# Optimization experiments

Hardware: AMD Instinct MI355X
Metric: run time of the kernel (lower is better)

Reference implementation:

```python
import jax, jax.numpy as jnp
import numpy as np
import math
from jax import lax

B, HS, WS, C, T, TD, HH, TOPM = 8, 64, 64, 512, 77, 512, 8, 3
DH = C // HH
CONF_TH = 0.35


def _layernorm(x, w, b, eps=1e-5):
    mu = x.mean(-1, keepdims=True)
    var = ((x - mu) ** 2).mean(-1, keepdims=True)
    return (x - mu) * lax.rsqrt(var + eps) * w + b


def _l2norm(x, eps=1e-6):
    n = jnp.sqrt((x * x).sum(-1, keepdims=True))
    return x / jnp.maximum(n, eps)


def _forward(visual_features, text_features, geo_mask,
             ln1_w, ln1_b, wq, bq, wk, bk, wv, bv, wo, bo,
             gate_w, gate_b, logit_scale, alpha,
             ln2_w, ln2_b, ffn_w1, ffn_b1, ffn_w2, ffn_b2):
    Bb, Hs, Ws, Cv = visual_features.shape
    N = Hs * Ws
    # Pre-LN + flatten spatial
    x = _layernorm(visual_features, ln1_w, ln1_b).reshape(Bb, N, Cv)
    q_full = x @ wq + bq                                  # [B,N,C]
    pad_mask = jnp.abs(text_features).sum(-1) <= 1e-6     # [B,T]
    k_full = text_features @ wk + bk                      # [B,T,C]
    v_full = text_features @ wv + bv
    # per-token L2 normalize over full channel dim, then split heads
    q = _l2norm(q_full).reshape(Bb, N, HH, DH)
    k = _l2norm(k_full).reshape(Bb, T, HH, DH)
    v = v_full.reshape(Bb, T, HH, DH)
    scale = jnp.exp(jnp.clip(logit_scale, -2.0, 2.0)) / jnp.sqrt(jnp.float32(DH))
    sim = jnp.einsum('bnhd,bthd->bnht', q, k) * scale     # [B,N,H,T]
    # geo gate (4D tensor branch): log-bias on logits + multiplicative channel gate later
    gate_map = jnp.clip(geo_mask, 0.3, 1.0)               # [B,1,Hs,Ws]
    geo_gate_flat = gate_map.reshape(Bb, N, 1)            # [B,N,1]
    sim = sim + jnp.log(jnp.maximum(gate_map.reshape(Bb, N), 1e-6))[:, :, None, None]
    sim = jnp.where(pad_mask[:, None, None, :], -jnp.inf, sim)
    # Top-K sparsification before softmax (threshold at the K-th value)
    topv = lax.top_k(sim, TOPM)[0]                        # [B,N,H,K]
    sim = jnp.where(sim >= topv[..., -1:], sim, -jnp.inf)
    attn = jax.nn.softmax(sim, axis=-1)
    attn = attn / jnp.maximum(attn.sum(-1, keepdims=True), 1e-6)
    # fully-padded rows -> zero
    all_pad = pad_mask.all(axis=1)
    attn = jnp.where(all_pad[:, None, None, None], 0.0, attn)
    # confidence bypass: conf = max_prob * (1 - normalized entropy), mean over heads
    a_hn = attn.transpose(0, 2, 1, 3)                     # [B,H,N,T]
    maxp = a_hn.max(-1, keepdims=True)
    t_eff = jnp.maximum((a_hn > 0).astype(a_hn.dtype).sum(-1, keepdims=True), 2.0)
    p = jnp.maximum(a_hn, 1e-8)
    ent = jnp.maximum(-(p * jnp.log(p)).sum(-1, keepdims=True) / jnp.log(t_eff), 0.0)
    conf = jnp.clip(maxp * (1.0 - ent), 0.0, 1.0).mean(axis=1)   # [B,N,1]
    conf_scale = CONF_TH + (1.0 - CONF_TH) * jnp.clip(conf, 0.0, 1.0)
    aligned = jnp.einsum('bnht,bthd->bnhd', attn, v).reshape(Bb, N, HH * DH)
    aligned = (aligned @ wo + bo) * conf_scale
    gate = jax.nn.sigmoid(x @ gate_w + gate_b) * geo_gate_flat
    y = x + alpha * gate * aligned
    h = _layernorm(y, ln2_w, ln2_b)
    y = y + (jax.nn.gelu(h @ ffn_w1 + ffn_b1, approximate=False) @ ffn_w2 + ffn_b2)
    return y.reshape(Bb, Hs, Ws, Cv)


def setup_inputs() -> dict:
    key = jax.random.key(0)
    ks = jax.random.split(key, 16)
    def w(k, shp, fan_in):
        return (jax.random.normal(k, shp, jnp.float32) * (1.0 / math.sqrt(fan_in))).astype(jnp.float32)
    return {
        'visual_features': jax.random.normal(ks[0], (B, HS, WS, C), jnp.float32),
        'text_features':   jax.random.normal(ks[1], (B, T, TD), jnp.float32),
        'geo_mask':        jax.random.uniform(ks[2], (B, 1, HS, WS), jnp.float32),
        'ln1_w': jnp.ones((C,), jnp.float32), 'ln1_b': jnp.zeros((C,), jnp.float32),
        'wq': w(ks[3], (C, C), C),   'bq': jnp.zeros((C,), jnp.float32),
        'wk': w(ks[4], (TD, C), TD), 'bk': jnp.zeros((C,), jnp.float32),
        'wv': w(ks[5], (TD, C), TD), 'bv': jnp.zeros((C,), jnp.float32),
        'wo': w(ks[6], (C, C), C),   'bo': jnp.zeros((C,), jnp.float32),
        'gate_w': w(ks[7], (C, C), C), 'gate_b': jnp.zeros((C,), jnp.float32),
        'logit_scale': jnp.float32(math.log(1.0 / 0.07)),
        'alpha': jnp.float32(0.1),
        'ln2_w': jnp.ones((C,), jnp.float32), 'ln2_b': jnp.zeros((C,), jnp.float32),
        'ffn_w1': w(ks[8], (C, 4 * C), C),    'ffn_b1': jnp.zeros((4 * C,), jnp.float32),
        'ffn_w2': w(ks[9], (4 * C, C), 4 * C), 'ffn_b2': jnp.zeros((C,), jnp.float32),
    }


def reference(visual_features, text_features, geo_mask,
              ln1_w, ln1_b, wq, bq, wk, bk, wv, bv, wo, bo,
              gate_w, gate_b, logit_scale, alpha,
              ln2_w, ln2_b, ffn_w1, ffn_b1, ffn_w2, ffn_b2):
    return _forward(visual_features, text_features, geo_mask,
                    ln1_w, ln1_b, wq, bq, wk, bk, wv, bv, wo, bo,
                    gate_w, gate_b, logit_scale, alpha,
                    ln2_w, ln2_b, ffn_w1, ffn_b1, ffn_w2, ffn_b2)
```

## Files before the change

### kernel.cpp

```cpp
#include <hip/hip_runtime.h>
#include <hip/hip_bf16.h>
#include <math.h>

#define TT 77
#define MTOT 32768

typedef __attribute__((ext_vector_type(8))) short bf16x8;
typedef __attribute__((ext_vector_type(4))) float floatx4;

#define GPTR(p) ((const __attribute__((address_space(1))) void*)(p))
#define LPTR(p) ((__attribute__((address_space(3))) void*)(p))

__device__ __forceinline__ float wred_sum(float v) {
#pragma unroll
  for (int o = 32; o >= 1; o >>= 1) v += __shfl_xor(v, o, 64);
  return v;
}

__device__ __forceinline__ unsigned short f2bf(float f) {
  unsigned int u = __float_as_uint(f);
  unsigned int r = (u + 0x7fffu + ((u >> 16) & 1u)) >> 16;
  return (unsigned short)r;
}
__device__ __forceinline__ float bf2f(unsigned short h) {
  return __uint_as_float(((unsigned int)h) << 16);
}
__device__ __forceinline__ unsigned int cvt2bf(float a, float b) {
  unsigned int r;
  asm("v_cvt_pk_bf16_f32 %0, %1, %2" : "=v"(r) : "v"(a), "v"(b));
  return r;
}

__device__ __forceinline__ float fast_gelu(float o) {
  const float z = fabsf(o) * 0.70710678118654752f;
  const float t = __builtin_amdgcn_rcpf(fmaf(0.3275911f, z, 1.0f));
  float p = fmaf(1.061405429f, t, -1.453152027f);
  p = fmaf(p, t, 1.421413741f);
  p = fmaf(p, t, -0.284496736f);
  p = fmaf(p, t, 0.254829592f);
  p = p * t;
  const float erfz = fmaf(-p, __expf(-z * z), 1.0f);
  const float s = __builtin_copysignf(erfz, o);
  return 0.5f * o * (1.0f + s);
}

__device__ __forceinline__ float fast_sigmoid(float o) {
  return __builtin_amdgcn_rcpf(1.0f + __expf(-o));
}

__global__ __launch_bounds__(256)
void ln_bf16_kernel(const float* __restrict__ in, const float* __restrict__ gw,
                    const float* __restrict__ gb, unsigned short* __restrict__ out) {
  const int wv = threadIdx.x >> 6, lane = threadIdx.x & 63;
  const size_t row = (size_t)blockIdx.x * 4 + wv;
  const float* p = in + row * 512 + lane * 8;
  float4 a = *(const float4*)p;
  float4 b = *(const float4*)(p + 4);
  float s = a.x + a.y + a.z + a.w + b.x + b.y + b.z + b.w;
  float mu = wred_sum(s) * (1.0f / 512.0f);
  float d[8] = {a.x - mu, a.y - mu, a.z - mu, a.w - mu,
                b.x - mu, b.y - mu, b.z - mu, b.w - mu};
  float ss = 0.f;
#pragma unroll
  for (int i = 0; i < 8; ++i) ss = fmaf(d[i], d[i], ss);
  float var = wred_sum(ss) * (1.0f / 512.0f);
  float rstd = rsqrtf(var + 1e-5f);
  float4 w0 = *(const float4*)(gw + lane * 8);
  float4 w1 = *(const float4*)(gw + lane * 8 + 4);
  float4 c0 = *(const float4*)(gb + lane * 8);
  float4 c1 = *(const float4*)(gb + lane * 8 + 4);
  float o[8];
  o[0] = d[0] * rstd * w0.x + c0.x;  o[1] = d[1] * rstd * w0.y + c0.y;
  o[2] = d[2] * rstd * w0.z + c0.z;  o[3] = d[3] * rstd * w0.w + c0.w;
  o[4] = d[4] * rstd * w1.x + c1.x;  o[5] = d[5] * rstd * w1.y + c1.y;
  o[6] = d[6] * rstd * w1.z + c1.z;  o[7] = d[7] * rstd * w1.w + c1.w;
  __align__(16) unsigned short ob[8];
#pragma unroll
  for (int i = 0; i < 8; ++i) ob[i] = f2bf(o[i]);
  *(uint4*)(out + row * 512 + lane * 8) = *(const uint4*)ob;
}

__global__ __launch_bounds__(256)
void zero_acc_kernel(float* __restrict__ ssq, float* __restrict__ conf) {
  const int i = blockIdx.x * 256 + threadIdx.x;
  ssq[i] = 0.0f;
  conf[i] = 0.0f;
}

__global__ __launch_bounds__(256)
void transpose_bf16_kernel(const float* __restrict__ W, unsigned short* __restrict__ WTb,
                           int K, int N) {
  __shared__ float s[32][33];
  const int tx = threadIdx.x & 31, ty = threadIdx.x >> 5;
  const int n0 = blockIdx.x * 32, k0 = blockIdx.y * 32;
#pragma unroll
  for (int j = 0; j < 4; ++j)
    s[ty + 8 * j][tx] = W[(size_t)(k0 + ty + 8 * j) * N + n0 + tx];
  __syncthreads();
#pragma unroll
  for (int j = 0; j < 4; ++j)
    WTb[(size_t)(n0 + ty + 8 * j) * K + k0 + tx] = f2bf(s[tx][ty + 8 * j]);
}

__global__ __launch_bounds__(256)
void transpose_pair_kernel(const float* __restrict__ W,
                           unsigned short* __restrict__ WTh,
                           unsigned short* __restrict__ WTl, int K, int N) {
  __shared__ float s[32][33];
  const int tx = threadIdx.x & 31, ty = threadIdx.x >> 5;
  const int n0 = blockIdx.x * 32, k0 = blockIdx.y * 32;
#pragma unroll
  for (int j = 0; j < 4; ++j)
    s[ty + 8 * j][tx] = W[(size_t)(k0 + ty + 8 * j) * N + n0 + tx];
  __syncthreads();
#pragma unroll
  for (int j = 0; j < 4; ++j) {
    const float a = s[tx][ty + 8 * j];
    const unsigned short hi = f2bf(a);
    WTh[(size_t)(n0 + ty + 8 * j) * K + k0 + tx] = hi;
    WTl[(size_t)(n0 + ty + 8 * j) * K + k0 + tx] = f2bf(a - bf2f(hi));
  }
}

__global__ __launch_bounds__(256)
void text_cvt_kernel(const float* __restrict__ text,
                     unsigned short* __restrict__ thi,
                     unsigned short* __restrict__ tlo,
                     float* __restrict__ negm) {
  const int wv = threadIdx.x >> 6, lane = threadIdx.x & 63;
  const int row = blockIdx.x * 4 + wv;
  if (row >= 616) {
    const uint4 z = {0u, 0u, 0u, 0u};
    *(uint4*)(thi + (size_t)row * 512 + lane * 8) = z;
    *(uint4*)(tlo + (size_t)row * 512 + lane * 8) = z;
    return;
  }
  const float* p = text + (size_t)row * 512 + lane * 8;
  float4 a = *(const float4*)p;
  float4 b = *(const float4*)(p + 4);
  float v[8] = {a.x, a.y, a.z, a.w, b.x, b.y, b.z, b.w};
  float ab = 0.f;
#pragma unroll
  for (int i = 0; i < 8; ++i) ab += fabsf(v[i]);
  ab = wred_sum(ab);
  __align__(16) unsigned short hb[8];
  __align__(16) unsigned short lb[8];
#pragma unroll
  for (int i = 0; i < 8; ++i) {
    hb[i] = f2bf(v[i]);
    lb[i] = f2bf(v[i] - bf2f(hb[i]));
  }
  *(uint4*)(thi + (size_t)row * 512 + lane * 8) = *(const uint4*)hb;
  *(uint4*)(tlo + (size_t)row * 512 + lane * 8) = *(const uint4*)lb;
  if (lane == 0) {
    const int bb = row / 77, t = row - bb * 77;
    negm[bb * 80 + t] = (ab <= 1e-6f) ? -INFINITY : 0.0f;
  }
}

__global__ __launch_bounds__(256)
void kv_gemm(const unsigned short* __restrict__ AH,
             const unsigned short* __restrict__ AL,
             const unsigned short* __restrict__ BH,
             const unsigned short* __restrict__ BL,
             const float* __restrict__ bk, const float* __restrict__ bv,
             float* __restrict__ outp) {
  const int K = 512;
  __shared__ __align__(16) unsigned short AsH[128 * 32];
  __shared__ __align__(16) unsigned short AsL[128 * 32];
  __shared__ __align__(16) unsigned short BsH[128 * 32];
  __shared__ __align__(16) unsigned short BsL[128 * 32];
  const int tid = threadIdx.x;
  const int wid = tid >> 6, lane = tid & 63;
  const int wr = wid >> 1, wc = wid & 1;
  const int m16 = lane & 15, quad = lane >> 4;
  const int row0 = blockIdx.y * 128, col0 = blockIdx.x * 128;

  const floatx4 zero4 = {0.f, 0.f, 0.f, 0.f};
  floatx4 acc[4][4];
#pragma unroll
  for (int i = 0; i < 4; ++i)
#pragma unroll
    for (int j = 0; j < 4; ++j) acc[i][j] = zero4;

  const int srow = tid >> 2;
  const int schunk = (tid & 3) ^ (srow & 3);
  const unsigned short* AgH = AH + (size_t)(row0 + srow) * K + schunk * 8;
  const unsigned short* AgL = AL + (size_t)(row0 + srow) * K + schunk * 8;
  const unsigned short* BgH = BH + (size_t)(col0 + srow) * K + schunk * 8;
  const unsigned short* BgL = BL + (size_t)(col0 + srow) * K + schunk * 8;
  char* AsHB = (char*)AsH + tid * 16;
  char* AsLB = (char*)AsL + tid * 16;
  char* BsHB = (char*)BsH + tid * 16;
  char* BsLB = (char*)BsL + tid * 16;
  const int rq = quad ^ (m16 & 3);
  const int aOfs = (wr * 64 + m16) * 32 + rq * 8;
  const int bOfs = (wc * 64 + m16) * 32 + rq * 8;

  for (int k0 = 0; k0 < K; k0 += 32) {
    __syncthreads();
    __builtin_amdgcn_global_load_lds(GPTR(AgH + k0), LPTR(AsHB), 16, 0, 0);
    __builtin_amdgcn_global_load_lds(GPTR(AgH + (size_t)64 * K + k0), LPTR(AsHB + 4096), 16, 0, 0);
    __builtin_amdgcn_global_load_lds(GPTR(AgL + k0), LPTR(AsLB), 16, 0, 0);
    __builtin_amdgcn_global_load_lds(GPTR(AgL + (size_t)64 * K + k0), LPTR(AsLB + 4096), 16, 0, 0);
    __builtin_amdgcn_global_load_lds(GPTR(BgH + k0), LPTR(BsHB), 16, 0, 0);
    __builtin_amdgcn_global_load_lds(GPTR(BgH + (size_t)64 * K + k0), LPTR(BsHB + 4096), 16, 0, 0);
    __builtin_amdgcn_global_load_lds(GPTR(BgL + k0), LPTR(BsLB), 16, 0, 0);
    __builtin_amdgcn_global_load_lds(GPTR(BgL + (size_t)64 * K + k0), LPTR(BsLB + 4096), 16, 0, 0);
    __syncthreads();
    bf16x8 afH[4], afL[4], bfH[4], bfL[4];
#pragma unroll
    for (int i = 0; i < 4; ++i) {
      afH[i] = *(const bf16x8*)(AsH + aOfs + i * 16 * 32);
      afL[i] = *(const bf16x8*)(AsL + aOfs + i * 16 * 32);
      bfH[i] = *(const bf16x8*)(BsH + bOfs + i * 16 * 32);
      bfL[i] = *(const bf16x8*)(BsL + bOfs + i * 16 * 32);
    }
#pragma unroll
    for (int mi = 0; mi < 4; ++mi)
#pragma unroll
      for (int ni = 0; ni < 4; ++ni) {
        acc[mi][ni] = __builtin_amdgcn_mfma_f32_16x16x32_bf16(afH[mi], bfH[ni], acc[mi][ni], 0, 0, 0);
        acc[mi][ni] = __builtin_amdgcn_mfma_f32_16x16x32_bf16(afH[mi], bfL[ni], acc[mi][ni], 0, 0, 0);
        acc[mi][ni] = __builtin_amdgcn_mfma_f32_16x16x32_bf16(afL[mi], bfH[ni], acc[mi][ni], 0, 0, 0);
      }
  }

  const float* bp = (col0 < 512) ? bk : bv;
  const int cbase = (col0 < 512) ? col0 : col0 - 512;
  float bb[4];
#pragma unroll
  for (int ni = 0; ni < 4; ++ni) bb[ni] = bp[cbase + wc * 64 + ni * 16 + m16];
#pragma unroll
  for (int mi = 0; mi < 4; ++mi)
#pragma unroll
    for (int r = 0; r < 4; ++r) {
      const int row = row0 + wr * 64 + mi * 16 + quad * 4 + r;
#pragma unroll
      for (int ni = 0; ni < 4; ++ni) {
        const int col = col0 + wc * 64 + ni * 16 + m16;
        outp[(size_t)row * 1024 + col] = acc[mi][ni][r] + bb[ni];
      }
    }
}

__global__ __launch_bounds__(256)
void knorm_kernel(const float* __restrict__ KV,
                  unsigned short* __restrict__ khb) {
  const int wv = threadIdx.x >> 6, lane = threadIdx.x & 63;
  const int row = blockIdx.x * 4 + wv;
  const float* p = KV + (size_t)row * 1024 + lane * 8;
  float4 a = *(const float4*)p;
  float4 b = *(const float4*)(p + 4);
  float v[8] = {a.x, a.y, a.z, a.w, b.x, b.y, b.z, b.w};
  float ss = 0.f;
#pragma unroll
  for (int i = 0; i < 8; ++i) ss = fmaf(v[i], v[i], ss);
  ss = wred_sum(ss);
  const float sc = 1.0f / fmaxf(sqrtf(ss), 1e-6f);
  const int bb = row / 77, t = row - bb * 77;
  const int c = lane * 8, h = c >> 6, d = c & 63;
  __align__(16) unsigned short ob[8];
#pragma unroll
  for (int i = 0; i < 8; ++i) ob[i] = f2bf(v[i] * sc);
  *(uint4*)(khb + (((size_t)bb * 8 + h) * 80 + t) * 64 + d) = *(const uint4*)ob;
}

__global__ __launch_bounds__(256)
void kpad_zero_kernel(unsigned short* __restrict__ khb, float* __restrict__ negm) {
  const int i = blockIdx.x * 256 + threadIdx.x;
  const int bh = i / 192, rem = i - bh * 192;
  const int t = 77 + rem / 64, d = rem & 63;
  khb[(((size_t)bh) * 80 + t) * 64 + d] = 0;
  if (i < 24) negm[(i / 3) * 80 + 77 + (i % 3)] = -INFINITY;
}

__global__ __launch_bounds__(256)
void sim_attn_kernel(const unsigned short* __restrict__ qnb,
                     const unsigned short* __restrict__ khb,
                     const float* __restrict__ negm,
                     const float* __restrict__ ssq,
                     const float* __restrict__ logit_scale,
                     const float* __restrict__ vf,
                     unsigned short* __restrict__ alignedb,
                     float* __restrict__ confacc) {
  __shared__ __align__(16) char lbuf[128 * 81 * 4];
  unsigned short* As = (unsigned short*)lbuf;
  unsigned short* Bs = As + 128 * 72;
  float* simt = (float*)lbuf;

  const int bh = blockIdx.y;
  const int b = bh >> 3, h = bh & 7;
  const int row0 = blockIdx.x * 128;
  const int tid = threadIdx.x;

  {
    const int r = tid >> 1, half = tid & 1;
    const unsigned short* src = qnb + ((size_t)b * 4096 + row0 + r) * 512 + h * 64 + half * 32;
    unsigned short* dst = As + r * 72 + half * 32;
    *(uint4*)dst = *(const uint4*)src;
    *(uint4*)(dst + 8) = *(const uint4*)(src + 8);
    *(uint4*)(dst + 16) = *(const uint4*)(src + 16);
    *(uint4*)(dst + 24) = *(const uint4*)(src + 24);
  }
  if (tid < 160) {
    const int r = tid >> 1, half = tid & 1;
    const unsigned short* src = khb + ((size_t)bh * 80 + r) * 64 + half * 32;
    unsigned short* dst = Bs + r * 72 + half * 32;
    *(uint4*)dst = *(const uint4*)src;
    *(uint4*)(dst + 8) = *(const uint4*)(src + 8);
    *(uint4*)(dst + 16) = *(const uint4*)(src + 16);
    *(uint4*)(dst + 24) = *(const uint4*)(src + 24);
  }
  __syncthreads();

  const int w = tid >> 6, lane = tid & 63;
  const int m16 = lane & 15, quad = lane >> 4;
  const unsigned short* aBase = As + (w * 32 + m16) * 72 + quad * 8;
  const unsigned short* bBase = Bs + m16 * 72 + quad * 8;
  bf16x8 af[2][2], bf[5][2];
#pragma unroll
  for (int mi = 0; mi < 2; ++mi)
#pragma unroll
    for (int kk = 0; kk < 2; ++kk)
      af[mi][kk] = *(const bf16x8*)(aBase + mi * 16 * 72 + kk * 32);
#pragma unroll
  for (int ni = 0; ni < 5; ++ni)
#pragma unroll
    for (int kk = 0; kk < 2; ++kk)
      bf[ni][kk] = *(const bf16x8*)(bBase + ni * 16 * 72 + kk * 32);
  __syncthreads();

  const floatx4 zero4 = {0.f, 0.f, 0.f, 0.f};
  floatx4 acc[2][5];
#pragma unroll
  for (int mi = 0; mi < 2; ++mi)
#pragma unroll
    for (int ni = 0; ni < 5; ++ni) acc[mi][ni] = zero4;
#pragma unroll
  for (int kk = 0; kk < 2; ++kk)
#pragma unroll
    for (int mi = 0; mi < 2; ++mi)
#pragma unroll
      for (int ni = 0; ni < 5; ++ni)
        acc[mi][ni] = __builtin_amdgcn_mfma_f32_16x16x32_bf16(af[mi][kk], bf[ni][kk], acc[mi][ni], 0, 0, 0);

  const float ls = fminf(fmaxf(logit_scale[0], -2.0f), 2.0f);
  const float scale = expf(ls) * 0.125f;
  float nm[5];
#pragma unroll
  for (int ni = 0; ni < 5; ++ni) nm[ni] = negm[b * 80 + ni * 16 + m16];
#pragma unroll
  for (int mi = 0; mi < 2; ++mi)
#pragma unroll
    for (int r = 0; r < 4; ++r) {
      const int lr = w * 32 + quad * 4 + mi * 16 + r;
      const float ssv = ssq[(size_t)b * 4096 + row0 + lr];
      const float nsc = scale / fmaxf(sqrtf(ssv), 1e-6f);
#pragma unroll
      for (int ni = 0; ni < 5; ++ni)
        simt[lr * 81 + ni * 16 + m16] = acc[mi][ni][r] * nsc + nm[ni];
    }
  __syncthreads();

  const int lr = tid >> 1, half = tid & 1;
  const int n = row0 + lr;
  const float* sp = simt + lr * 81;

  float m1 = -INFINITY, m2 = -INFINITY, m3 = -INFINITY, m4 = -INFINITY;
  int a1 = 0, a2 = 0, a3 = 0;
  for (int t = 0; t < 80; ++t) {
    const float v = sp[t];
    const bool c1 = v > m1, c2 = v > m2, c3 = v > m3, c4 = v > m4;
    m4 = c4 ? (c3 ? m3 : v) : m4;
    m3 = c3 ? (c2 ? m2 : v) : m3;
    a3 = c3 ? (c2 ? a2 : t) : a3;
    m2 = c2 ? (c1 ? m1 : v) : m2;
    a2 = c2 ? (c1 ? a1 : t) : a2;
    m1 = c1 ? v : m1;
    a1 = c1 ? t : a1;
  }

  const bool dead = (m1 == -INFINITY);
  if (dead) m1 = 0.0f;
  const bool tie = (!dead) && ((m1 == m2) || (m2 == m3) || (m3 == m4));

  const float d2 = m2 - m1, d3 = m3 - m1;
  const float e2 = __expf(d2), e3 = __expf(d3);
  float s0 = 1.0f + e2 + e3;
  float s1 = ((e2 > 0.f) ? e2 * d2 : 0.f) + ((e3 > 0.f) ? e3 * d3 : 0.f);
  float cntf = 1.0f + ((e2 > 0.f) ? 1.f : 0.f) + ((e3 > 0.f) ? 1.f : 0.f);

  unsigned short* op = alignedb + ((size_t)b * 4096 + n) * 512 + h * 64 + half * 32;

  if (tie) {
    s0 = 0.f; s1 = 0.f; cntf = 0.f;
    float4 acc2[8];
#pragma unroll
    for (int i = 0; i < 8; ++i) acc2[i] = (float4){0.f, 0.f, 0.f, 0.f};
    for (int t = 0; t < 80; ++t) {
      const float v = sp[t];
      if (v >= m3) {
        const float e = expf(v - m1);
        if (e > 0.f) {
          s0 += e; s1 = fmaf(e, v - m1, s1); cntf += 1.f;
          const float4* vp = (const float4*)(vf + (size_t)(b * 77 + t) * 1024 + h * 64 + half * 32);
#pragma unroll
          for (int i = 0; i < 8; ++i) {
            const float4 x = vp[i];
            acc2[i].x = fmaf(e, x.x, acc2[i].x);
            acc2[i].y = fmaf(e, x.y, acc2[i].y);
            acc2[i].z = fmaf(e, x.z, acc2[i].z);
            acc2[i].w = fmaf(e, x.w, acc2[i].w);
          }
        }
      }
    }
    const float invt = 1.0f / s0;
#pragma unroll
    for (int i = 0; i < 4; ++i) {
      const float4 lo = acc2[2 * i], hi = acc2[2 * i + 1];
      uint4 pk;
      pk.x = cvt2bf(lo.x * invt, lo.y * invt);
      pk.y = cvt2bf(lo.z * invt, lo.w * invt);
      pk.z = cvt2bf(hi.x * invt, hi.y * invt);
      pk.w = cvt2bf(hi.z * invt, hi.w * invt);
      *(uint4*)(op + i * 8) = pk;
    }
  } else {
    const float inv0 = 1.0f / s0;
    const float wA = dead ? 0.f : inv0;
    const float wB = e2 * inv0, wC = e3 * inv0;
    const float* v1p = vf + (size_t)(b * 77 + a1) * 1024 + h * 64 + half * 32;
    const float* v2p = vf + (size_t)(b * 77 + a2) * 1024 + h * 64 + half * 32;
    const float* v3p = vf + (size_t)(b * 77 + a3) * 1024 + h * 64 + half * 32;
#pragma unroll
    for (int i = 0; i < 4; ++i) {
      const float4 x0 = ((const float4*)v1p)[2 * i];
      const float4 x1 = ((const float4*)v1p)[2 * i + 1];
      const float4 y0 = ((const float4*)v2p)[2 * i];
      const float4 y1 = ((const float4*)v2p)[2 * i + 1];
      const float4 z0 = ((const float4*)v3p)[2 * i];
      const float4 z1 = ((const float4*)v3p)[2 * i + 1];
      float4 r0, r1;
      r0.x = fmaf(wC, z0.x, fmaf(wB, y0.x, wA * x0.x));
      r0.y = fmaf(wC, z0.y, fmaf(wB, y0.y, wA * x0.y));
      r0.z = fmaf(wC, z0.z, fmaf(wB, y0.z, wA * x0.z));
      r0.w = fmaf(wC, z0.w, fmaf(wB, y0.w, wA * x0.w));
      r1.x = fmaf(wC, z1.x, fmaf(wB, y1.x, wA * x1.x));
      r1.y = fmaf(wC, z1.y, fmaf(wB, y1.y, wA * x1.y));
      r1.z = fmaf(wC, z1.z, fmaf(wB, y1.z, wA * x1.z));
      r1.w = fmaf(wC, z1.w, fmaf(wB, y1.w, wA * x1.w));
      uint4 pk;
      pk.x = cvt2bf(r0.x, r0.y);
      pk.y = cvt2bf(r0.z, r0.w);
      pk.z = cvt2bf(r1.x, r1.y);
      pk.w = cvt2bf(r1.z, r1.w);
      *(uint4*)(op + i * 8) = pk;
    }
  }

  if (half == 0) {
    const float inv = 1.0f / s0;
    const float entn = (__logf(s0) - s1 * inv) + (77.0f - cntf) * 1.8420681e-7f;
    const float ent = fmaxf(entn / __logf(fmaxf(cntf, 2.0f)), 0.0f);
    float conf_h = fminf(fmaxf(inv * (1.0f - ent), 0.0f), 1.0f);
    if (dead) conf_h = 0.f;
    atomicAdd(confacc + (size_t)b * 4096 + n, conf_h * 0.125f);
  }
}

template <int EPI, int KC>
__global__ __launch_bounds__(256)
void mfma_gemm(const unsigned short* __restrict__ A,
               const unsigned short* __restrict__ WT,
               const float* __restrict__ bias,
               void* __restrict__ outv, int M, int N,
               const unsigned short* __restrict__ e0b,
               const float* __restrict__ e1f,
               const float* __restrict__ e2f,
               const float* __restrict__ scf) {
  __shared__ __align__(16) unsigned short As[2][128 * 64];
  __shared__ __align__(16) unsigned short Bs[2][128 * 64];
  const int tid = threadIdx.x;
  const int wid = tid >> 6, lane = tid & 63;
  const int wr = wid >> 1, wc = wid & 1;
  const int m16 = lane & 15, quad = lane >> 4;

  const int nwg = gridDim.x * gridDim.y;
  const int orig = blockIdx.y * gridDim.x + blockIdx.x;
  const int qq = nwg >> 3, rr = nwg & 7;
  const int xcd = orig & 7, base = orig >> 3;
  const int logical = (xcd < rr ? xcd * (qq + 1) : rr * (qq + 1) + (xcd - rr) * qq) + base;
  const int bx = logical % gridDim.x, by = logical / gridDim.x;
  const int row0 = by * 128, col0 = bx * 128;

  const floatx4 zero4 = {0.f, 0.f, 0.f, 0.f};
  floatx4 acc[4][4];
#pragma unroll
  for (int i = 0; i < 4; ++i)
#pragma unroll
    for (int j = 0; j < 4; ++j) acc[i][j] = zero4;

  size_t aoff[4], boff[4];
  unsigned int ldso[4];
#pragma unroll
  for (int j = 0; j < 4; ++j) {
    const int s = wid * 64 + j * 256 + lane;
    const int r = s >> 3;
    const int gc = (s & 7) ^ (r & 7);
    aoff[j] = (size_t)(row0 + r) * KC + gc * 8;
    const int br = (r & 64) + 4 * (r & 15) + ((r >> 4) & 3);
    boff[j] = (size_t)(col0 + br) * KC + gc * 8;
    ldso[j] = (unsigned int)s * 16;
  }

  constexpr int NT = KC / 64;
#pragma unroll
  for (int j = 0; j < 4; ++j) {
    __builtin_amdgcn_global_load_lds(GPTR(A + aoff[j]), LPTR((char*)As[0] + ldso[j]), 16, 0, 0);
    __builtin_amdgcn_global_load_lds(GPTR(WT + boff[j]), LPTR((char*)Bs[0] + ldso[j]), 16, 0, 0);
  }
  __syncthreads();

  int cur = 0;
  for (int t = 0; t < NT; ++t) {
    if (t + 1 < NT) {
      const size_t k0n = (size_t)(t + 1) * 64;
#pragma unroll
      for (int j = 0; j < 4; ++j) {
        __builtin_amdgcn_global_load_lds(GPTR(A + aoff[j] + k0n), LPTR((char*)As[cur ^ 1] + ldso[j]), 16, 0, 0);
        __builtin_amdgcn_global_load_lds(GPTR(WT + boff[j] + k0n), LPTR((char*)Bs[cur ^ 1] + ldso[j]), 16, 0, 0);
      }
    }
#pragma unroll
    for (int kk = 0; kk < 2; ++kk) {
      const int pc = (kk * 4 + quad) ^ (m16 & 7);
      bf16x8 af[4], bfr[4];
#pragma unroll
      for (int i = 0; i < 4; ++i) {
        af[i] = *(const bf16x8*)((const char*)As[cur] + (wr * 64 + i * 16 + m16) * 128 + pc * 16);
        bfr[i] = *(const bf16x8*)((const char*)Bs[cur] + (wc * 64 + i * 16 + m16) * 128 + pc * 16);
      }
#pragma unroll
      for (int mi = 0; mi < 4; ++mi)
#pragma unroll
        for (int ni = 0; ni < 4; ++ni)
          acc[mi][ni] = __builtin_amdgcn_mfma_f32_16x16x32_bf16(af[mi], bfr[ni], acc[mi][ni], 0, 0, 0);
    }
    if (t + 1 < NT) {
      __syncthreads();
      cur ^= 1;
    }
  }

  float* outf = (float*)outv;
  unsigned short* outb = (unsigned short*)outv;
  const unsigned short* albf = (const unsigned short*)e1f;
  const int colb = col0 + wc * 64 + 4 * m16;
  const float4 bbv = *(const float4*)(bias + colb);
  const float bb[4] = {bbv.x, bbv.y, bbv.z, bbv.w};
  const float alphav = (EPI == 2) ? scf[0] : 0.f;

#pragma unroll
  for (int mi = 0; mi < 4; ++mi) {
#pragma unroll
    for (int r = 0; r < 4; ++r) {
      const int row = row0 + wr * 64 + mi * 16 + quad * 4 + r;
      float o[4];
#pragma unroll
      for (int ni = 0; ni < 4; ++ni) o[ni] = acc[mi][ni][r] + bb[ni];
      const size_t basei = (size_t)row * N + colb;

      if (EPI == 5) {
        uint2 pk;
        pk.x = cvt2bf(o[0], o[1]);
        pk.y = cvt2bf(o[2], o[3]);
        *(uint2*)(outb + basei) = pk;
        float p = fmaf(o[0], o[0], fmaf(o[1], o[1], fmaf(o[2], o[2], o[3] * o[3])));
        p += __shfl_xor(p, 1, 64);
        p += __shfl_xor(p, 2, 64);
        p += __shfl_xor(p, 4, 64);
        p += __shfl_xor(p, 8, 64);
        if (m16 == 0) atomicAdd(const_cast<float*>(e1f) + row, p);
      } else if (EPI == 3) {
        uint2 pk;
        pk.x = cvt2bf(fast_gelu(o[0]), fast_gelu(o[1]));
        pk.y = cvt2bf(fast_gelu(o[2]), fast_gelu(o[3]));
        *(uint2*)(outb + basei) = pk;
      } else if (EPI == 1) {
        const float cm = fminf(fmaxf(e1f[row], 0.0f), 1.0f);
        const float rowscale = 0.35f + 0.65f * cm;
        uint2 pk;
        pk.x = cvt2bf(o[0] * rowscale, o[1] * rowscale);
        pk.y = cvt2bf(o[2] * rowscale, o[3] * rowscale);
        *(uint2*)(outb + basei) = pk;
      } else if (EPI == 2) {
        const float geo = fminf(fmaxf(e2f[row], 0.3f), 1.0f);
        const uint2 xpk = *(const uint2*)(e0b + basei);
        const uint2 apk = *(const uint2*)(albf + basei);
        const float xv[4] = {bf2f((unsigned short)xpk.x), bf2f((unsigned short)(xpk.x >> 16)),
                             bf2f((unsigned short)xpk.y), bf2f((unsigned short)(xpk.y >> 16))};
        const float av[4] = {bf2f((unsigned short)apk.x), bf2f((unsigned short)(apk.x >> 16)),
                             bf2f((unsigned short)apk.y), bf2f((unsigned short)(apk.y >> 16))};
        float4 ov;
        ov.x = xv[0] + alphav * fast_sigmoid(o[0]) * geo * av[0];
        ov.y = xv[1] + alphav * fast_sigmoid(o[1]) * geo * av[1];
        ov.z = xv[2] + alphav * fast_sigmoid(o[2]) * geo * av[2];
        ov.w = xv[3] + alphav * fast_sigmoid(o[3]) * geo * av[3];
        *(float4*)(outf + basei) = ov;
      } else {
        const float4 rv = *(const float4*)(e1f + basei);
        float4 ov;
        ov.x = o[0] + rv.x;
        ov.y = o[1] + rv.y;
        ov.z = o[2] + rv.z;
        ov.w = o[3] + rv.w;
        *(float4*)(outf + basei) = ov;
      }
    }
  }
}

extern "C" void kernel_launch(void* const* d_in, const int* in_sizes, int n_in,
                              void* d_out, int out_size, void* d_ws, size_t ws_size,
                              hipStream_t stream) {
  const float* visual = (const float*)d_in[0];
  const float* text   = (const float*)d_in[1];
  const float* geo    = (const float*)d_in[2];
  const float* ln1_w  = (const float*)d_in[3];
  const float* ln1_b  = (const float*)d_in[4];
  const float* wq     = (const float*)d_in[5];
  const float* bq     = (const float*)d_in[6];
  const float* wk     = (const float*)d_in[7];
  const float* bk     = (const float*)d_in[8];
  const float* wvw    = (const float*)d_in[9];
  const float* bv     = (const float*)d_in[10];
  const float* wo     = (const float*)d_in[11];
  const float* bo     = (const float*)d_in[12];
  const float* gate_w = (const float*)d_in[13];
  const float* gate_b = (const float*)d_in[14];
  const float* logit_scale = (const float*)d_in[15];
  const float* alpha  = (const float*)d_in[16];
  const float* ln2_w  = (const float*)d_in[17];
  const float* ln2_b  = (const float*)d_in[18];
  const float* ffn_w1 = (const float*)d_in[19];
  const float* ffn_b1 = (const float*)d_in[20];
  const float* ffn_w2 = (const float*)d_in[21];
  const float* ffn_b2 = (const float*)d_in[22];
  float* out = (float*)d_out;

  char* ws = (char*)d_ws;
  float* R0            = (float*)ws;
  float* BUF2          = (float*)(ws + 88080384);
  unsigned short* Xb   = (unsigned short*)(ws + 155189248);
  unsigned short* QNb  = (unsigned short*)(ws + 188743680);
  unsigned short* wqT  = (unsigned short*)(ws + 222298112);
  unsigned short* woT  = wqT + 262144;
  unsigned short* gateT = woT + 262144;
  unsigned short* w1T  = gateT + 262144;
  unsigned short* w2T  = w1T + 1048576;
  unsigned short* KHb  = w2T + 1048576;
  float* NEGM = (float*)(ws + 230146048);
  float* CONF = (float*)(ws + 230148608);
  float* SSQ  = (float*)(ws + 230279680);

  float* KV            = (float*)(ws + 88080384);
  unsigned short* THi  = (unsigned short*)(ws + 88080384 + 2621440);
  unsigned short* TLo  = THi + 640 * 512;
  unsigned short* WKVh = TLo + 640 * 512;
  unsigned short* WKVl = WKVh + 1024 * 512;

  unsigned short* ALb = (unsigned short*)R0;
  unsigned short* AOb = QNb;

  transpose_bf16_kernel<<<dim3(16, 16), 256, 0, stream>>>(wq, wqT, 512, 512);
  transpose_bf16_kernel<<<dim3(16, 16), 256, 0, stream>>>(wo, woT, 512, 512);
  transpose_bf16_kernel<<<dim3(16, 16), 256, 0, stream>>>(gate_w, gateT, 512, 512);
  transpose_bf16_kernel<<<dim3(64, 16), 256, 0, stream>>>(ffn_w1, w1T, 512, 2048);
  transpose_bf16_kernel<<<dim3(16, 64), 256, 0, stream>>>(ffn_w2, w2T, 2048, 512);
  transpose_pair_kernel<<<dim3(16, 16), 256, 0, stream>>>(wk, WKVh, WKVl, 512, 512);
  transpose_pair_kernel<<<dim3(16, 16), 256, 0, stream>>>(wvw, WKVh + 512 * 512, WKVl + 512 * 512, 512, 512);

  ln_bf16_kernel<<<MTOT / 4, 256, 0, stream>>>(visual, ln1_w, ln1_b, Xb);
  zero_acc_kernel<<<128, 256, 0, stream>>>(SSQ, CONF);
  text_cvt_kernel<<<160, 256, 0, stream>>>(text, THi, TLo, NEGM);
  kv_gemm<<<dim3(8, 5), 256, 0, stream>>>(THi, TLo, WKVh, WKVl, bk, bv, KV);
  knorm_kernel<<<154, 256, 0, stream>>>(KV, KHb);
  kpad_zero_kernel<<<48, 256, 0, stream>>>(KHb, NEGM);
  mfma_gemm<5, 512><<<dim3(4, 256), 256, 0, stream>>>(Xb, wqT, bq, QNb, MTOT, 512,
                                                      nullptr, SSQ, nullptr, nullptr);
  sim_attn_kernel<<<dim3(32, 64), 256, 0, stream>>>(QNb, KHb, NEGM, SSQ, logit_scale,
                                                    KV + 512, ALb, CONF);
  mfma_gemm<1, 512><<<dim3(4, 256), 256, 0, stream>>>(ALb, woT, bo, AOb, MTOT, 512,
                                                      nullptr, CONF, nullptr, nullptr);
  mfma_gemm<2, 512><<<dim3(4, 256), 256, 0, stream>>>(Xb, gateT, gate_b, BUF2, MTOT, 512,
                                                      Xb, (const float*)AOb, geo, alpha);
  ln_bf16_kernel<<<MTOT / 4, 256, 0, stream>>>(BUF2, ln2_w, ln2_b, Xb);
  unsigned short* GCH = (unsigned short*)R0;
  for (int ch = 0; ch < 2; ++ch) {
    const size_t off = (size_t)ch * 16384;
    mfma_gemm<3, 512><<<dim3(16, 128), 256, 0, stream>>>(Xb + off * 512, w1T, ffn_b1, GCH,
                                                         16384, 2048,
                                                         nullptr, nullptr, nullptr, nullptr);
    mfma_gemm<4, 2048><<<dim3(4, 128), 256, 0, stream>>>(GCH, w2T, ffn_b2, out + off * 512,
                                                         16384, 512,
                                                         nullptr, BUF2 + off * 512, nullptr, nullptr);
  }
}
```

Measured before the change: 625.1 us.

## Single-buffer default GEMM, add BK=32 double-buffered path for FFN1, vectorize top-k scan

The default GEMM path now uses one 64-wide K buffer with two barriers per step, so it no longer overlaps the next tile's loads with compute. This halves LDS use (16 KB per block) to raise occupancy. A new PIPE variant, used only by the FFN up-projection, double-buffers 32-wide K tiles with a 4-chunk swizzle in the same 16 KB. The attention kernel pads its sim rows to 84 floats so the top-k scan can use float4 LDS loads in a fully unrolled loop. The trade is occupancy against lost overlap in the non-pipelined GEMMs.

```diff
diff --git a/kernel.cpp b/kernel.cpp
--- a/kernel.cpp
+++ b/kernel.cpp
@@ -284,7 +284,7 @@
                      const float* __restrict__ vf,
                      unsigned short* __restrict__ alignedb,
                      float* __restrict__ confacc) {
-  __shared__ __align__(16) char lbuf[128 * 81 * 4];
+  __shared__ __align__(16) char lbuf[128 * 84 * 4];
   unsigned short* As = (unsigned short*)lbuf;
   unsigned short* Bs = As + 128 * 72;
   float* simt = (float*)lbuf;
@@ -359,26 +359,32 @@
       const float nsc = scale / fmaxf(sqrtf(ssv), 1e-6f);
 #pragma unroll
       for (int ni = 0; ni < 5; ++ni)
-        simt[lr * 81 + ni * 16 + m16] = acc[mi][ni][r] * nsc + nm[ni];
+        simt[lr * 84 + ni * 16 + m16] = acc[mi][ni][r] * nsc + nm[ni];
     }
   __syncthreads();
 
   const int lr = tid >> 1, half = tid & 1;
   const int n = row0 + lr;
-  const float* sp = simt + lr * 81;
+  const float* sp = simt + lr * 84;
 
   float m1 = -INFINITY, m2 = -INFINITY, m3 = -INFINITY, m4 = -INFINITY;
   int a1 = 0, a2 = 0, a3 = 0;
-  for (int t = 0; t < 80; ++t) {
-    const float v = sp[t];
-    const bool c1 = v > m1, c2 = v > m2, c3 = v > m3, c4 = v > m4;
-    m4 = c4 ? (c3 ? m3 : v) : m4;
-    m3 = c3 ? (c2 ? m2 : v) : m3;
-    a3 = c3 ? (c2 ? a2 : t) : a3;
-    m2 = c2 ? (c1 ? m1 : v) : m2;
-    a2 = c2 ? (c1 ? a1 : t) : a2;
-    m1 = c1 ? v : m1;
-    a1 = c1 ? t : a1;
+#pragma unroll
+  for (int i = 0; i < 20; ++i) {
+    const float4 q4 = ((const float4*)sp)[i];
+#pragma unroll
+    for (int j = 0; j < 4; ++j) {
+      const float v = (j == 0) ? q4.x : (j == 1) ? q4.y : (j == 2) ? q4.z : q4.w;
+      const int t = i * 4 + j;
+      const bool c1 = v > m1, c2 = v > m2, c3 = v > m3, c4 = v > m4;
+      m4 = c4 ? (c3 ? m3 : v) : m4;
+      m3 = c3 ? (c2 ? m2 : v) : m3;
+      a3 = c3 ? (c2 ? a2 : t) : a3;
+      m2 = c2 ? (c1 ? m1 : v) : m2;
+      a2 = c2 ? (c1 ? a1 : t) : a2;
+      m1 = c1 ? v : m1;
+      a1 = c1 ? t : a1;
+    }
   }
 
   const bool dead = (m1 == -INFINITY);
@@ -470,7 +476,7 @@
   }
 }
 
-template <int EPI, int KC>
+template <int EPI, int KC, bool PIPE = false>
 __global__ __launch_bounds__(256)
 void mfma_gemm(const unsigned short* __restrict__ A,
                const unsigned short* __restrict__ WT,
@@ -480,8 +486,8 @@
                const float* __restrict__ e1f,
                const float* __restrict__ e2f,
                const float* __restrict__ scf) {
-  __shared__ __align__(16) unsigned short As[2][128 * 64];
-  __shared__ __align__(16) unsigned short Bs[2][128 * 64];
+  __shared__ __align__(16) unsigned short As[8192];
+  __shared__ __align__(16) unsigned short Bs[8192];
   const int tid = threadIdx.x;
   const int wid = tid >> 6, lane = tid & 63;
   const int wr = wid >> 1, wc = wid & 1;
@@ -502,55 +508,93 @@
 #pragma unroll
     for (int j = 0; j < 4; ++j) acc[i][j] = zero4;
 
-  size_t aoff[4], boff[4];
-  unsigned int ldso[4];
-#pragma unroll
-  for (int j = 0; j < 4; ++j) {
-    const int s = wid * 64 + j * 256 + lane;
-    const int r = s >> 3;
-    const int gc = (s & 7) ^ (r & 7);
-    aoff[j] = (size_t)(row0 + r) * KC + gc * 8;
-    const int br = (r & 64) + 4 * (r & 15) + ((r >> 4) & 3);
-    boff[j] = (size_t)(col0 + br) * KC + gc * 8;
-    ldso[j] = (unsigned int)s * 16;
-  }
-
-  constexpr int NT = KC / 64;
-#pragma unroll
-  for (int j = 0; j < 4; ++j) {
-    __builtin_amdgcn_global_load_lds(GPTR(A + aoff[j]), LPTR((char*)As[0] + ldso[j]), 16, 0, 0);
-    __builtin_amdgcn_global_load_lds(GPTR(WT + boff[j]), LPTR((char*)Bs[0] + ldso[j]), 16, 0, 0);
-  }
-  __syncthreads();
-
-  int cur = 0;
-  for (int t = 0; t < NT; ++t) {
-    if (t + 1 < NT) {
-      const size_t k0n = (size_t)(t + 1) * 64;
+  if constexpr (!PIPE) {
+    size_t aoff[4], boff[4];
+    unsigned int ldso[4];
+#pragma unroll
+    for (int j = 0; j < 4; ++j) {
+      const int s = wid * 64 + j * 256 + lane;
+      const int r = s >> 3;
+      const int gc = (s & 7) ^ (r & 7);
+      aoff[j] = (size_t)(row0 + r) * KC + gc * 8;
+      const int br = (r & 64) + 4 * (r & 15) + ((r >> 4) & 3);
+      boff[j] = (size_t)(col0 + br) * KC + gc * 8;
+      ldso[j] = (unsigned int)s * 16;
+    }
+    for (int k0 = 0; k0 < KC; k0 += 64) {
+      __syncthreads();
 #pragma unroll
       for (int j = 0; j < 4; ++j) {
-        __builtin_amdgcn_global_load_lds(GPTR(A + aoff[j] + k0n), LPTR((char*)As[cur ^ 1] + ldso[j]), 16, 0, 0);
-        __builtin_amdgcn_global_load_lds(GPTR(WT + boff[j] + k0n), LPTR((char*)Bs[cur ^ 1] + ldso[j]), 16, 0, 0);
-      }
-    }
-#pragma unroll
-    for (int kk = 0; kk < 2; ++kk) {
-      const int pc = (kk * 4 + quad) ^ (m16 & 7);
-      bf16x8 af[4], bfr[4];
-#pragma unroll
-      for (int i = 0; i < 4; ++i) {
-        af[i] = *(const bf16x8*)((const char*)As[cur] + (wr * 64 + i * 16 + m16) * 128 + pc * 16);
-        bfr[i] = *(const bf16x8*)((const char*)Bs[cur] + (wc * 64 + i * 16 + m16) * 128 + pc * 16);
-      }
-#pragma unroll
-      for (int mi = 0; mi < 4; ++mi)
-#pragma unroll
-        for (int ni = 0; ni < 4; ++ni)
-          acc[mi][ni] = __builtin_amdgcn_mfma_f32_16x16x32_bf16(af[mi], bfr[ni], acc[mi][ni], 0, 0, 0);
-    }
-    if (t + 1 < NT) {
+        __builtin_amdgcn_global_load_lds(GPTR(A + aoff[j] + k0), LPTR((char*)As + ldso[j]), 16, 0, 0);
+        __builtin_amdgcn_global_load_lds(GPTR(WT + boff[j] + k0), LPTR((char*)Bs + ldso[j]), 16, 0, 0);
+      }
       __syncthreads();
-      cur ^= 1;
+#pragma unroll
+      for (int kk = 0; kk < 2; ++kk) {
+        const int pc = (kk * 4 + quad) ^ (m16 & 7);
+        bf16x8 af[4], bfr[4];
+#pragma unroll
+        for (int i = 0; i < 4; ++i) {
+          af[i] = *(const bf16x8*)((const char*)As + (wr * 64 + i * 16 + m16) * 128 + pc * 16);
+          bfr[i] = *(const bf16x8*)((const char*)Bs + (wc * 64 + i * 16 + m16) * 128 + pc * 16);
+        }
+#pragma unroll
+        for (int mi = 0; mi < 4; ++mi)
+#pragma unroll
+          for (int ni = 0; ni < 4; ++ni)
+            acc[mi][ni] = __builtin_amdgcn_mfma_f32_16x16x32_bf16(af[mi], bfr[ni], acc[mi][ni], 0, 0, 0);
+      }
+    }
+  } else {
+    size_t aoff[2], boff[2];
+    unsigned int ldso[2];
+#pragma unroll
+    for (int j = 0; j < 2; ++j) {
+      const int s = j * 256 + tid;
+      const int r = s >> 2;
+      const int gc = (s & 3) ^ (r & 3);
+      aoff[j] = (size_t)(row0 + r) * KC + gc * 8;
+      const int br = (r & 64) + 4 * (r & 15) + ((r >> 4) & 3);
+      boff[j] = (size_t)(col0 + br) * KC + gc * 8;
+      ldso[j] = (unsigned int)s * 16;
+    }
+    const int rq = quad ^ (m16 & 3);
+    const int NT = KC / 32;
+#pragma unroll
+    for (int j = 0; j < 2; ++j) {
+      __builtin_amdgcn_global_load_lds(GPTR(A + aoff[j]), LPTR((char*)As + ldso[j]), 16, 0, 0);
+      __builtin_amdgcn_global_load_lds(GPTR(WT + boff[j]), LPTR((char*)Bs + ldso[j]), 16, 0, 0);
+    }
+    __syncthreads();
+    int cur = 0;
+    for (int t = 0; t < NT; ++t) {
+      if (t + 1 < NT) {
+        const size_t k0n = (size_t)(t + 1) * 32;
+        const unsigned int bofs = (unsigned int)(cur ^ 1) * 8192;
+#pragma unroll
+        for (int j = 0; j < 2; ++j) {
+          __builtin_amdgcn_global_load_lds(GPTR(A + aoff[j] + k0n), LPTR((char*)As + bofs + ldso[j]), 16, 0, 0);
+          __builtin_amdgcn_global_load_lds(GPTR(WT + boff[j] + k0n), LPTR((char*)Bs + bofs + ldso[j]), 16, 0, 0);
+        }
+      }
+      {
+        const unsigned int cofs = (unsigned int)cur * 8192;
+        bf16x8 af[4], bfr[4];
+#pragma unroll
+        for (int i = 0; i < 4; ++i) {
+          af[i] = *(const bf16x8*)((const char*)As + cofs + (wr * 64 + i * 16 + m16) * 64 + rq * 16);
+          bfr[i] = *(const bf16x8*)((const char*)Bs + cofs + (wc * 64 + i * 16 + m16) * 64 + rq * 16);
+        }
+#pragma unroll
+        for (int mi = 0; mi < 4; ++mi)
+#pragma unroll
+          for (int ni = 0; ni < 4; ++ni)
+            acc[mi][ni] = __builtin_amdgcn_mfma_f32_16x16x32_bf16(af[mi], bfr[ni], acc[mi][ni], 0, 0, 0);
+      }
+      if (t + 1 < NT) {
+        __syncthreads();
+        cur ^= 1;
+      }
     }
   }
 
@@ -700,9 +744,9 @@
   unsigned short* GCH = (unsigned short*)R0;
   for (int ch = 0; ch < 2; ++ch) {
     const size_t off = (size_t)ch * 16384;
-    mfma_gemm<3, 512><<<dim3(16, 128), 256, 0, stream>>>(Xb + off * 512, w1T, ffn_b1, GCH,
-                                                         16384, 2048,
-                                                         nullptr, nullptr, nullptr, nullptr);
+    mfma_gemm<3, 512, true><<<dim3(16, 128), 256, 0, stream>>>(Xb + off * 512, w1T, ffn_b1, GCH,
+                                                               16384, 2048,
+                                                               nullptr, nullptr, nullptr, nullptr);
     mfma_gemm<4, 2048><<<dim3(4, 128), 256, 0, stream>>>(GCH, w2T, ffn_b2, out + off * 512,
                                                          16384, 512,
                                                          nullptr, BUF2 + off * 512, nullptr, nullptr);
```

Result: faster. 578.3 us (-7.5%).
